# Kernel optimization log

Hardware: AMD Instinct MI355X
Metric: run time of the kernel (lower is better)

Reference implementation:

```python
import jax, jax.numpy as jnp
import numpy as np

H = 1024
F = 3584
E = 8
TOP_K = 2
B, S = 2, 1024


def setup_inputs() -> dict:
    key = jax.random.key(0)
    ks = jax.random.split(key, 5)
    scale_h = 1.0 / np.sqrt(H)
    scale_f = 1.0 / np.sqrt(F)
    return {
        "hidden_states": jax.random.normal(ks[0], (B, S, H), dtype=jnp.float32),
        "gate_w": jax.random.normal(ks[1], (H, E), dtype=jnp.float32) * scale_h,
        "w1": jax.random.normal(ks[2], (E, H, F), dtype=jnp.float32) * scale_h,
        "w3": jax.random.normal(ks[3], (E, H, F), dtype=jnp.float32) * scale_h,
        "w2": jax.random.normal(ks[4], (E, F, H), dtype=jnp.float32) * scale_f,
        "top_k": TOP_K,
    }


def reference(hidden_states, gate_w, w1, w3, w2, top_k):
    b, s, h = hidden_states.shape
    e = gate_w.shape[1]
    x = hidden_states.reshape(-1, h)  # [N, H]

    # Router: softmax over experts, top-k selection, renormalize (Mixtral).
    logits = x @ gate_w                             # [N, E]
    probs = jax.nn.softmax(logits, axis=-1)
    rw, sel = jax.lax.top_k(probs, top_k)           # [N, K]
    rw = rw / jnp.sum(rw, axis=-1, keepdims=True)

    # Dispatch/combine weights: combine[n, e] = sum_k rw[n,k] * (sel[n,k]==e).
    # This is the mathematical equivalent of moe_permute + weighted moe_unpermute.
    combine = jnp.sum(jax.nn.one_hot(sel, e, dtype=rw.dtype) * rw[..., None], axis=1)  # [N, E]

    # Grouped SwiGLU expert MLPs; loop over the small fixed expert count so the
    # [N, F] intermediate is materialized one expert at a time.
    out = jnp.zeros_like(x)
    for ei in range(e):
        hdn = jax.nn.silu(x @ w1[ei]) * (x @ w3[ei])  # [N, F]
        out = out + combine[:, ei:ei + 1] * (hdn @ w2[ei])
    return out.reshape(b, s, h)
```

## Files before the change

### kernel.cpp

```cpp
#include <hip/hip_runtime.h>
#include <hip/hip_bf16.h>

#define NTOK 2048
#define HD   1024
#define FD   3584
#define NE   8

#define BM 128
#define BN1 64
#define BN 128
#define BK 64
#define NIT1 (HD / BK)
#define KS2 4
#define KLEN2 (FD / KS2)
#define NIT2 (KLEN2 / BK)

typedef __attribute__((ext_vector_type(8))) short short8;
typedef __attribute__((ext_vector_type(4))) float f32x4;

__device__ __forceinline__ unsigned short f2bf(float f) {
    __hip_bfloat16 h = __float2bfloat16(f);
    union { __hip_bfloat16 h; unsigned short u; } c; c.h = h;
    return c.u;
}

typedef __attribute__((address_space(1))) const unsigned int g_cu32;
typedef __attribute__((address_space(3))) unsigned int l_u32;
__device__ __forceinline__ void gl16(const void* g, void* l) {
    __builtin_amdgcn_global_load_lds((g_cu32*)g, (l_u32*)(unsigned int)(size_t)l, 16, 0, 0);
}

__global__ void k_router(const float* __restrict__ x, const float* __restrict__ gw,
                         int* __restrict__ sel, float* __restrict__ selw,
                         int* __restrict__ counts) {
    int token = blockIdx.x * 4 + (threadIdx.x >> 6);
    int lane  = threadIdx.x & 63;
    if (token >= NTOK) return;
    const float* xr = x + (size_t)token * HD;
    float acc[NE];
#pragma unroll
    for (int e = 0; e < NE; e++) acc[e] = 0.f;
    for (int h = lane; h < HD; h += 64) {
        float xv = xr[h];
        const float4* g = (const float4*)(gw + (size_t)h * NE);
        float4 g0 = g[0], g1 = g[1];
        acc[0] += xv * g0.x; acc[1] += xv * g0.y; acc[2] += xv * g0.z; acc[3] += xv * g0.w;
        acc[4] += xv * g1.x; acc[5] += xv * g1.y; acc[6] += xv * g1.z; acc[7] += xv * g1.w;
    }
#pragma unroll
    for (int e = 0; e < NE; e++) {
#pragma unroll
        for (int off = 32; off >= 1; off >>= 1) acc[e] += __shfl_xor(acc[e], off, 64);
    }
    if (lane == 0) {
        float m = acc[0];
#pragma unroll
        for (int e = 1; e < NE; e++) m = fmaxf(m, acc[e]);
        float z[NE];
#pragma unroll
        for (int e = 0; e < NE; e++) z[e] = expf(acc[e] - m);
        int e0 = 0; float z0 = z[0];
#pragma unroll
        for (int e = 1; e < NE; e++) if (z[e] > z0) { z0 = z[e]; e0 = e; }
        int e1 = -1; float z1 = -1.f;
#pragma unroll
        for (int e = 0; e < NE; e++) if (e != e0 && z[e] > z1) { z1 = z[e]; e1 = e; }
        float s = z0 + z1;
        sel[token * 2 + 0] = e0; sel[token * 2 + 1] = e1;
        selw[token * 2 + 0] = z0 / s; selw[token * 2 + 1] = z1 / s;
        atomicAdd(&counts[e0], 1);
        atomicAdd(&counts[e1], 1);
    }
}

__global__ void k_scan(const int* __restrict__ counts, int* __restrict__ basep,
                       int* __restrict__ fillc) {
    if (threadIdx.x == 0 && blockIdx.x == 0) {
        int b = 0;
        for (int e = 0; e < NE; e++) { basep[e] = b; b += counts[e]; fillc[e] = 0; }
    }
}

__global__ void k_fill(const int* __restrict__ sel, const float* __restrict__ selw,
                       const int* __restrict__ basep, int* __restrict__ fillc,
                       int* __restrict__ rowmap, int* __restrict__ rowk,
                       float* __restrict__ roww) {
    int n = blockIdx.x * blockDim.x + threadIdx.x;
    if (n >= NTOK) return;
#pragma unroll
    for (int k = 0; k < 2; k++) {
        int e = sel[n * 2 + k];
        int p = atomicAdd(&fillc[e], 1);
        int g = basep[e] + p;
        rowmap[g] = n; rowk[g] = k; roww[g] = selw[n * 2 + k];
    }
}

__global__ void k_cvt(const float* __restrict__ x, unsigned short* __restrict__ xb) {
    size_t i = ((size_t)blockIdx.x * blockDim.x + threadIdx.x) * 8;
    float4 a = *(const float4*)(x + i);
    float4 b = *(const float4*)(x + i + 4);
    unsigned short p[8] __attribute__((aligned(16))) =
        { f2bf(a.x), f2bf(a.y), f2bf(a.z), f2bf(a.w),
          f2bf(b.x), f2bf(b.y), f2bf(b.z), f2bf(b.w) };
    *(uint4*)(xb + i) = *(uint4*)p;
}

__global__ void k_wt(const float* __restrict__ w, unsigned short* __restrict__ wt,
                     int K, int N) {
    __shared__ unsigned short tile[64][66];
    const int t = threadIdx.x;
    const float* src = w + (size_t)blockIdx.z * K * N + ((size_t)blockIdx.y * 64) * N + blockIdx.x * 64;
    {
        const int r = t >> 4;
        const int c4 = (t & 15) * 4;
#pragma unroll
        for (int i = 0; i < 4; i++) {
            const int kr = r + i * 16;
            float4 v = *(const float4*)(src + (size_t)kr * N + c4);
            unsigned short p[4] = { f2bf(v.x), f2bf(v.y), f2bf(v.z), f2bf(v.w) };
            *(unsigned int*)&tile[kr][c4]     = *(unsigned int*)&p[0];
            *(unsigned int*)&tile[kr][c4 + 2] = *(unsigned int*)&p[2];
        }
    }
    __syncthreads();
    unsigned short* dst = wt + (size_t)blockIdx.z * N * K + ((size_t)blockIdx.x * 64) * K + blockIdx.y * 64;
    const int n = t >> 3;
    const int kc = (t & 7) * 8;
#pragma unroll
    for (int i = 0; i < 2; i++) {
        const int nn = n + i * 32;
        unsigned short p[8] __attribute__((aligned(16)));
#pragma unroll
        for (int j = 0; j < 8; j++) p[j] = tile[kc + j][nn];
        *(uint4*)&dst[(size_t)nn * K + kc] = *(uint4*)p;
    }
}

__global__ __launch_bounds__(512, 4) void k_gemm1(
    const unsigned short* __restrict__ xb,
    const unsigned short* __restrict__ w1t, const unsigned short* __restrict__ w3t,
    const int* __restrict__ counts, const int* __restrict__ basep,
    const int* __restrict__ rowmap, unsigned short* __restrict__ act)
{
    const int e = blockIdx.z;
    const int nrows = counts[e];
    const int m0 = blockIdx.y * BM;
    if (m0 >= nrows) return;
    const int f0 = blockIdx.x * BN1;
    const int gbase = basep[e];

    __shared__ __align__(16) unsigned short At[2][BM][BK];
    __shared__ __align__(16) unsigned short B1[2][BN1][BK];
    __shared__ __align__(16) unsigned short B3[2][BN1][BK];

    const int t = threadIdx.x;
    const int lane = t & 63;
    const int w = t >> 6;
    const int wrm = w >> 1, wnn = w & 1;
    const int lr = lane >> 3;
    const int so = ((lane & 7) ^ lr) * 8;

    const unsigned short* asrc[2];
#pragma unroll
    for (int c = 0; c < 2; c++) {
        const int row = (w * 2 + c) * 8 + lr;
        const int tok = rowmap[gbase + min(m0 + row, nrows - 1)];
        asrc[c] = xb + (size_t)tok * HD + so;
    }
    const int brow = w * 8 + lr;
    const unsigned short* b1src = w1t + ((size_t)(e * FD + f0 + brow)) * HD + so;
    const unsigned short* b3src = w3t + ((size_t)(e * FD + f0 + brow)) * HD + so;

    f32x4 acc1[2][2], acc3[2][2];
#pragma unroll
    for (int i = 0; i < 2; i++)
#pragma unroll
        for (int j = 0; j < 2; j++) { acc1[i][j] = (f32x4)(0.f); acc3[i][j] = (f32x4)(0.f); }

    const int l15 = lane & 15;
    const int lhi = lane >> 4;
    const int rs = (l15 & 7) * 8;

#pragma unroll
    for (int c = 0; c < 2; c++) gl16(asrc[c], &At[0][(w * 2 + c) * 8][0]);
    gl16(b1src, &B1[0][w * 8][0]);
    gl16(b3src, &B3[0][w * 8][0]);

    for (int it = 0; it < NIT1; ++it) {
        const int cur = it & 1;
        if (it + 1 < NIT1) {
            const int kn = (it + 1) * BK;
#pragma unroll
            for (int c = 0; c < 2; c++) gl16(asrc[c] + kn, &At[cur ^ 1][(w * 2 + c) * 8][0]);
            gl16(b1src + kn, &B1[cur ^ 1][w * 8][0]);
            gl16(b3src + kn, &B3[cur ^ 1][w * 8][0]);
            asm volatile("s_waitcnt vmcnt(4)" ::: "memory");
        } else {
            asm volatile("s_waitcnt vmcnt(0)" ::: "memory");
        }
        __builtin_amdgcn_s_barrier();
#pragma unroll
        for (int kk = 0; kk < 2; kk++) {
            const int kc = (kk * 32 + lhi * 8) ^ rs;
            short8 af[2], b1f[2], b3f[2];
#pragma unroll
            for (int i = 0; i < 2; i++)
                af[i] = *(const short8*)&At[cur][wrm * 32 + i * 16 + l15][kc];
#pragma unroll
            for (int j = 0; j < 2; j++) {
                b1f[j] = *(const short8*)&B1[cur][wnn * 32 + j * 16 + l15][kc];
                b3f[j] = *(const short8*)&B3[cur][wnn * 32 + j * 16 + l15][kc];
            }
#pragma unroll
            for (int i = 0; i < 2; i++)
#pragma unroll
                for (int j = 0; j < 2; j++) {
                    acc1[i][j] = __builtin_amdgcn_mfma_f32_16x16x32_bf16(af[i], b1f[j], acc1[i][j], 0, 0, 0);
                    acc3[i][j] = __builtin_amdgcn_mfma_f32_16x16x32_bf16(af[i], b3f[j], acc3[i][j], 0, 0, 0);
                }
        }
        __builtin_amdgcn_s_barrier();
    }

    const int rbase = wrm * 32 + lhi * 4;
    const int cbase = f0 + wnn * 32 + l15;
#pragma unroll
    for (int i = 0; i < 2; i++) {
#pragma unroll
        for (int r = 0; r < 4; r++) {
            const int ml = rbase + i * 16 + r;
            if (m0 + ml < nrows) {
                const size_t rowoff = (size_t)(gbase + m0 + ml) * FD;
#pragma unroll
                for (int j = 0; j < 2; j++) {
                    float y1 = acc1[i][j][r];
                    float y3 = acc3[i][j][r];
                    float sv = (y1 / (1.f + __expf(-y1))) * y3;
                    act[rowoff + cbase + j * 16] = f2bf(sv);
                }
            }
        }
    }
}

__global__ __launch_bounds__(512, 4) void k_gemm2(
    const unsigned short* __restrict__ act,
    const unsigned short* __restrict__ w2t,
    const int* __restrict__ counts, const int* __restrict__ basep,
    const int* __restrict__ rowmap, const int* __restrict__ rowk,
    const float* __restrict__ roww, float* __restrict__ partial)
{
    const int z = blockIdx.z;
    const int e = z >> 2, ks = z & 3;
    const int nrows = counts[e];
    const int m0 = blockIdx.y * BM;
    if (m0 >= nrows) return;
    const int h0 = blockIdx.x * BN;
    const int gbase = basep[e];
    const int kbase = ks * KLEN2;

    __shared__ __align__(16) unsigned short At[2][BM][BK];
    __shared__ __align__(16) unsigned short Bt[2][BN][BK];

    const int t = threadIdx.x;
    const int lane = t & 63;
    const int w = t >> 6;
    const int wr = w >> 2, wn = w & 3;
    const int lr = lane >> 3;
    const int so = ((lane & 7) ^ lr) * 8;

    const unsigned short* asrc[2];
    const unsigned short* bsrc[2];
#pragma unroll
    for (int c = 0; c < 2; c++) {
        const int row = (w * 2 + c) * 8 + lr;
        asrc[c] = act + ((size_t)gbase + min(m0 + row, nrows - 1)) * FD + so + kbase;
        bsrc[c] = w2t + ((size_t)(e * HD + h0 + row)) * FD + so + kbase;
    }

    f32x4 acc[4][2];
#pragma unroll
    for (int i = 0; i < 4; i++)
#pragma unroll
        for (int j = 0; j < 2; j++) acc[i][j] = (f32x4)(0.f);

    const int l15 = lane & 15;
    const int lhi = lane >> 4;
    const int rs = (l15 & 7) * 8;

#pragma unroll
    for (int c = 0; c < 2; c++) {
        gl16(asrc[c], &At[0][(w * 2 + c) * 8][0]);
        gl16(bsrc[c], &Bt[0][(w * 2 + c) * 8][0]);
    }

    for (int it = 0; it < NIT2; ++it) {
        const int cur = it & 1;
        if (it + 1 < NIT2) {
            const int kn = (it + 1) * BK;
#pragma unroll
            for (int c = 0; c < 2; c++) {
                gl16(asrc[c] + kn, &At[cur ^ 1][(w * 2 + c) * 8][0]);
                gl16(bsrc[c] + kn, &Bt[cur ^ 1][(w * 2 + c) * 8][0]);
            }
            asm volatile("s_waitcnt vmcnt(4)" ::: "memory");
        } else {
            asm volatile("s_waitcnt vmcnt(0)" ::: "memory");
        }
        __builtin_amdgcn_s_barrier();
#pragma unroll
        for (int kk = 0; kk < 2; kk++) {
            const int kc = (kk * 32 + lhi * 8) ^ rs;
            short8 af[4], bf[2];
#pragma unroll
            for (int i = 0; i < 4; i++)
                af[i] = *(const short8*)&At[cur][wr * 64 + i * 16 + l15][kc];
#pragma unroll
            for (int j = 0; j < 2; j++)
                bf[j] = *(const short8*)&Bt[cur][wn * 32 + j * 16 + l15][kc];
#pragma unroll
            for (int i = 0; i < 4; i++)
#pragma unroll
                for (int j = 0; j < 2; j++)
                    acc[i][j] = __builtin_amdgcn_mfma_f32_16x16x32_bf16(af[i], bf[j], acc[i][j], 0, 0, 0);
        }
        __builtin_amdgcn_s_barrier();
    }

    const int rbase = wr * 64 + lhi * 4;
    const int cbase = h0 + wn * 32 + l15;
#pragma unroll
    for (int i = 0; i < 4; i++) {
#pragma unroll
        for (int r = 0; r < 4; r++) {
            const int ml = rbase + i * 16 + r;
            if (m0 + ml < nrows) {
                const int grow = gbase + m0 + ml;
                const int tok = rowmap[grow];
                const int slot = rowk[grow];
                const float wv = roww[grow];
                float* op = partial + (((size_t)slot * KS2 + ks) * NTOK + tok) * HD + cbase;
#pragma unroll
                for (int j = 0; j < 2; j++) op[j * 16] = acc[i][j][r] * wv;
            }
        }
    }
}

__global__ void k_combine(const float* __restrict__ partial, float* __restrict__ out) {
    size_t i = ((size_t)blockIdx.x * blockDim.x + threadIdx.x) * 4;
    const size_t st = (size_t)NTOK * HD;
    float4 o = *(const float4*)(partial + i);
#pragma unroll
    for (int s = 1; s < 2 * KS2; s++) {
        float4 v = *(const float4*)(partial + (size_t)s * st + i);
        o.x += v.x; o.y += v.y; o.z += v.z; o.w += v.w;
    }
    *(float4*)(out + i) = o;
}

extern "C" void kernel_launch(void* const* d_in, const int* in_sizes, int n_in,
                              void* d_out, int out_size, void* d_ws, size_t ws_size,
                              hipStream_t stream) {
    const float* x  = (const float*)d_in[0];
    const float* gw = (const float*)d_in[1];
    const float* w1 = (const float*)d_in[2];
    const float* w3 = (const float*)d_in[3];
    const float* w2 = (const float*)d_in[4];
    float* out = (float*)d_out;

    char* ws = (char*)d_ws;
    size_t off = 0;
    auto alloc = [&](size_t b) { char* p = ws + off; off += (b + 255) & ~(size_t)255; return p; };
    int*   sel    = (int*)  alloc((size_t)NTOK * 2 * 4);
    float* selw   = (float*)alloc((size_t)NTOK * 2 * 4);
    int*   counts = (int*)  alloc(NE * 4);
    int*   basep  = (int*)  alloc(NE * 4);
    int*   fillc  = (int*)  alloc(NE * 4);
    int*   rowmap = (int*)  alloc((size_t)NTOK * 2 * 4);
    int*   rowk   = (int*)  alloc((size_t)NTOK * 2 * 4);
    float* roww   = (float*)alloc((size_t)NTOK * 2 * 4);
    unsigned short* xb  = (unsigned short*)alloc((size_t)NTOK * HD * 2);
    unsigned short* act = (unsigned short*)alloc((size_t)NTOK * 2 * FD * 2);
    unsigned short* w1t = (unsigned short*)alloc((size_t)NE * HD * FD * 2);
    unsigned short* w3t = (unsigned short*)alloc((size_t)NE * HD * FD * 2);
    unsigned short* w2t = (unsigned short*)alloc((size_t)NE * HD * FD * 2);
    float* partial = (float*)w1t;

    hipMemsetAsync(counts, 0, NE * 4, stream);
    k_wt<<<dim3(FD / 64, HD / 64, NE), 256, 0, stream>>>(w1, w1t, HD, FD);
    k_wt<<<dim3(FD / 64, HD / 64, NE), 256, 0, stream>>>(w3, w3t, HD, FD);
    k_wt<<<dim3(HD / 64, FD / 64, NE), 256, 0, stream>>>(w2, w2t, FD, HD);
    k_cvt<<<(NTOK * HD) / (256 * 8), 256, 0, stream>>>(x, xb);
    k_router<<<NTOK / 4, 256, 0, stream>>>(x, gw, sel, selw, counts);
    k_scan<<<1, 64, 0, stream>>>(counts, basep, fillc);
    k_fill<<<NTOK / 256, 256, 0, stream>>>(sel, selw, basep, fillc, rowmap, rowk, roww);
    k_gemm1<<<dim3(FD / BN1, NTOK / BM, NE), 512, 0, stream>>>(xb, w1t, w3t, counts, basep, rowmap, act);
    k_gemm2<<<dim3(HD / BN, NTOK / BM, NE * KS2), 512, 0, stream>>>(act, w2t, counts, basep, rowmap, rowk, roww, partial);
    k_combine<<<(NTOK * HD) / (256 * 4), 256, 0, stream>>>(partial, out);
}
```

Measured before the change: 340.0 us.

## Retile both MoE GEMMs for 256-thread blocks, halve split-K, fuse weight transposes

The three weight transpose/convert launches are merged into one kernel that picks w1, w3 or w2 from blockIdx.z. gemm1 now runs 256-thread blocks, with each wave covering 64 rows instead of 32. That gives it more MFMA work per wave and more reuse of each A/B fragment, at the cost of more accumulator registers. gemm2 uses a 64-row M tile, 64-column per-wave N tiles and split-K of 2 instead of 4. This halves the partial buffers that are written and then summed in the combine kernel, but each block gets a longer K loop and there are fewer blocks to spread across the device.

```diff
diff --git a/kernel.cpp b/kernel.cpp
--- a/kernel.cpp
+++ b/kernel.cpp
@@ -8,10 +8,11 @@
 
 #define BM 128
 #define BN1 64
+#define BM2 64
 #define BN 128
 #define BK 64
 #define NIT1 (HD / BK)
-#define KS2 4
+#define KS2 2
 #define KLEN2 (FD / KS2)
 #define NIT2 (KLEN2 / BK)
 
@@ -106,11 +107,32 @@
     *(uint4*)(xb + i) = *(uint4*)p;
 }
 
-__global__ void k_wt(const float* __restrict__ w, unsigned short* __restrict__ wt,
-                     int K, int N) {
+__global__ void k_wt3(const float* __restrict__ w1, const float* __restrict__ w3,
+                      const float* __restrict__ w2,
+                      unsigned short* __restrict__ w1t, unsigned short* __restrict__ w3t,
+                      unsigned short* __restrict__ w2t) {
     __shared__ unsigned short tile[64][66];
+    const int z = blockIdx.z;
+    int K, N, tx, ty;
+    const float* src;
+    unsigned short* dst;
+    if (z < 16) {
+        K = HD; N = FD;
+        const int e = z & 7;
+        src = (z < 8 ? w1 : w3) + (size_t)e * K * N;
+        dst = (z < 8 ? w1t : w3t) + (size_t)e * N * K;
+        tx = blockIdx.x % (FD / 64); ty = blockIdx.x / (FD / 64);
+    } else {
+        K = FD; N = HD;
+        const int e = z - 16;
+        src = w2 + (size_t)e * K * N;
+        dst = w2t + (size_t)e * N * K;
+        tx = blockIdx.x % (HD / 64); ty = blockIdx.x / (HD / 64);
+    }
+    src += (size_t)(ty * 64) * N + tx * 64;
+    dst += (size_t)(tx * 64) * K + ty * 64;
+
     const int t = threadIdx.x;
-    const float* src = w + (size_t)blockIdx.z * K * N + ((size_t)blockIdx.y * 64) * N + blockIdx.x * 64;
     {
         const int r = t >> 4;
         const int c4 = (t & 15) * 4;
@@ -124,7 +146,6 @@
         }
     }
     __syncthreads();
-    unsigned short* dst = wt + (size_t)blockIdx.z * N * K + ((size_t)blockIdx.x * 64) * K + blockIdx.y * 64;
     const int n = t >> 3;
     const int kc = (t & 7) * 8;
 #pragma unroll
@@ -137,7 +158,7 @@
     }
 }
 
-__global__ __launch_bounds__(512, 4) void k_gemm1(
+__global__ __launch_bounds__(256, 2) void k_gemm1(
     const unsigned short* __restrict__ xb,
     const unsigned short* __restrict__ w1t, const unsigned short* __restrict__ w3t,
     const int* __restrict__ counts, const int* __restrict__ basep,
@@ -161,20 +182,25 @@
     const int lr = lane >> 3;
     const int so = ((lane & 7) ^ lr) * 8;
 
-    const unsigned short* asrc[2];
+    const unsigned short* asrc[4];
+#pragma unroll
+    for (int c = 0; c < 4; c++) {
+        const int row = (w * 4 + c) * 8 + lr;
+        const int tok = rowmap[gbase + min(m0 + row, nrows - 1)];
+        asrc[c] = xb + (size_t)tok * HD + so;
+    }
+    const unsigned short* b1src[2];
+    const unsigned short* b3src[2];
 #pragma unroll
     for (int c = 0; c < 2; c++) {
         const int row = (w * 2 + c) * 8 + lr;
-        const int tok = rowmap[gbase + min(m0 + row, nrows - 1)];
-        asrc[c] = xb + (size_t)tok * HD + so;
-    }
-    const int brow = w * 8 + lr;
-    const unsigned short* b1src = w1t + ((size_t)(e * FD + f0 + brow)) * HD + so;
-    const unsigned short* b3src = w3t + ((size_t)(e * FD + f0 + brow)) * HD + so;
-
-    f32x4 acc1[2][2], acc3[2][2];
-#pragma unroll
-    for (int i = 0; i < 2; i++)
+        b1src[c] = w1t + ((size_t)(e * FD + f0 + row)) * HD + so;
+        b3src[c] = w3t + ((size_t)(e * FD + f0 + row)) * HD + so;
+    }
+
+    f32x4 acc1[4][2], acc3[4][2];
+#pragma unroll
+    for (int i = 0; i < 4; i++)
 #pragma unroll
         for (int j = 0; j < 2; j++) { acc1[i][j] = (f32x4)(0.f); acc3[i][j] = (f32x4)(0.f); }
 
@@ -183,19 +209,25 @@
     const int rs = (l15 & 7) * 8;
 
 #pragma unroll
-    for (int c = 0; c < 2; c++) gl16(asrc[c], &At[0][(w * 2 + c) * 8][0]);
-    gl16(b1src, &B1[0][w * 8][0]);
-    gl16(b3src, &B3[0][w * 8][0]);
+    for (int c = 0; c < 4; c++) gl16(asrc[c], &At[0][(w * 4 + c) * 8][0]);
+#pragma unroll
+    for (int c = 0; c < 2; c++) {
+        gl16(b1src[c], &B1[0][(w * 2 + c) * 8][0]);
+        gl16(b3src[c], &B3[0][(w * 2 + c) * 8][0]);
+    }
 
     for (int it = 0; it < NIT1; ++it) {
         const int cur = it & 1;
         if (it + 1 < NIT1) {
             const int kn = (it + 1) * BK;
 #pragma unroll
-            for (int c = 0; c < 2; c++) gl16(asrc[c] + kn, &At[cur ^ 1][(w * 2 + c) * 8][0]);
-            gl16(b1src + kn, &B1[cur ^ 1][w * 8][0]);
-            gl16(b3src + kn, &B3[cur ^ 1][w * 8][0]);
-            asm volatile("s_waitcnt vmcnt(4)" ::: "memory");
+            for (int c = 0; c < 4; c++) gl16(asrc[c] + kn, &At[cur ^ 1][(w * 4 + c) * 8][0]);
+#pragma unroll
+            for (int c = 0; c < 2; c++) {
+                gl16(b1src[c] + kn, &B1[cur ^ 1][(w * 2 + c) * 8][0]);
+                gl16(b3src[c] + kn, &B3[cur ^ 1][(w * 2 + c) * 8][0]);
+            }
+            asm volatile("s_waitcnt vmcnt(8)" ::: "memory");
         } else {
             asm volatile("s_waitcnt vmcnt(0)" ::: "memory");
         }
@@ -203,17 +235,17 @@
 #pragma unroll
         for (int kk = 0; kk < 2; kk++) {
             const int kc = (kk * 32 + lhi * 8) ^ rs;
-            short8 af[2], b1f[2], b3f[2];
-#pragma unroll
-            for (int i = 0; i < 2; i++)
-                af[i] = *(const short8*)&At[cur][wrm * 32 + i * 16 + l15][kc];
+            short8 af[4], b1f[2], b3f[2];
+#pragma unroll
+            for (int i = 0; i < 4; i++)
+                af[i] = *(const short8*)&At[cur][wrm * 64 + i * 16 + l15][kc];
 #pragma unroll
             for (int j = 0; j < 2; j++) {
                 b1f[j] = *(const short8*)&B1[cur][wnn * 32 + j * 16 + l15][kc];
                 b3f[j] = *(const short8*)&B3[cur][wnn * 32 + j * 16 + l15][kc];
             }
 #pragma unroll
-            for (int i = 0; i < 2; i++)
+            for (int i = 0; i < 4; i++)
 #pragma unroll
                 for (int j = 0; j < 2; j++) {
                     acc1[i][j] = __builtin_amdgcn_mfma_f32_16x16x32_bf16(af[i], b1f[j], acc1[i][j], 0, 0, 0);
@@ -223,10 +255,10 @@
         __builtin_amdgcn_s_barrier();
     }
 
-    const int rbase = wrm * 32 + lhi * 4;
+    const int rbase = wrm * 64 + lhi * 4;
     const int cbase = f0 + wnn * 32 + l15;
 #pragma unroll
-    for (int i = 0; i < 2; i++) {
+    for (int i = 0; i < 4; i++) {
 #pragma unroll
         for (int r = 0; r < 4; r++) {
             const int ml = rbase + i * 16 + r;
@@ -244,7 +276,7 @@
     }
 }
 
-__global__ __launch_bounds__(512, 4) void k_gemm2(
+__global__ __launch_bounds__(256, 4) void k_gemm2(
     const unsigned short* __restrict__ act,
     const unsigned short* __restrict__ w2t,
     const int* __restrict__ counts, const int* __restrict__ basep,
@@ -252,59 +284,61 @@
     const float* __restrict__ roww, float* __restrict__ partial)
 {
     const int z = blockIdx.z;
-    const int e = z >> 2, ks = z & 3;
+    const int e = z >> 1, ks = z & 1;
     const int nrows = counts[e];
-    const int m0 = blockIdx.y * BM;
+    const int m0 = blockIdx.y * BM2;
     if (m0 >= nrows) return;
     const int h0 = blockIdx.x * BN;
     const int gbase = basep[e];
     const int kbase = ks * KLEN2;
 
-    __shared__ __align__(16) unsigned short At[2][BM][BK];
+    __shared__ __align__(16) unsigned short At[2][BM2][BK];
     __shared__ __align__(16) unsigned short Bt[2][BN][BK];
 
     const int t = threadIdx.x;
     const int lane = t & 63;
     const int w = t >> 6;
-    const int wr = w >> 2, wn = w & 3;
+    const int wr2 = w >> 1, wn2 = w & 1;
     const int lr = lane >> 3;
     const int so = ((lane & 7) ^ lr) * 8;
 
     const unsigned short* asrc[2];
-    const unsigned short* bsrc[2];
 #pragma unroll
     for (int c = 0; c < 2; c++) {
         const int row = (w * 2 + c) * 8 + lr;
         asrc[c] = act + ((size_t)gbase + min(m0 + row, nrows - 1)) * FD + so + kbase;
+    }
+    const unsigned short* bsrc[4];
+#pragma unroll
+    for (int c = 0; c < 4; c++) {
+        const int row = (w * 4 + c) * 8 + lr;
         bsrc[c] = w2t + ((size_t)(e * HD + h0 + row)) * FD + so + kbase;
     }
 
-    f32x4 acc[4][2];
-#pragma unroll
-    for (int i = 0; i < 4; i++)
-#pragma unroll
-        for (int j = 0; j < 2; j++) acc[i][j] = (f32x4)(0.f);
+    f32x4 acc[2][4];
+#pragma unroll
+    for (int i = 0; i < 2; i++)
+#pragma unroll
+        for (int j = 0; j < 4; j++) acc[i][j] = (f32x4)(0.f);
 
     const int l15 = lane & 15;
     const int lhi = lane >> 4;
     const int rs = (l15 & 7) * 8;
 
 #pragma unroll
-    for (int c = 0; c < 2; c++) {
-        gl16(asrc[c], &At[0][(w * 2 + c) * 8][0]);
-        gl16(bsrc[c], &Bt[0][(w * 2 + c) * 8][0]);
-    }
+    for (int c = 0; c < 2; c++) gl16(asrc[c], &At[0][(w * 2 + c) * 8][0]);
+#pragma unroll
+    for (int c = 0; c < 4; c++) gl16(bsrc[c], &Bt[0][(w * 4 + c) * 8][0]);
 
     for (int it = 0; it < NIT2; ++it) {
         const int cur = it & 1;
         if (it + 1 < NIT2) {
             const int kn = (it + 1) * BK;
 #pragma unroll
-            for (int c = 0; c < 2; c++) {
-                gl16(asrc[c] + kn, &At[cur ^ 1][(w * 2 + c) * 8][0]);
-                gl16(bsrc[c] + kn, &Bt[cur ^ 1][(w * 2 + c) * 8][0]);
-            }
-            asm volatile("s_waitcnt vmcnt(4)" ::: "memory");
+            for (int c = 0; c < 2; c++) gl16(asrc[c] + kn, &At[cur ^ 1][(w * 2 + c) * 8][0]);
+#pragma unroll
+            for (int c = 0; c < 4; c++) gl16(bsrc[c] + kn, &Bt[cur ^ 1][(w * 4 + c) * 8][0]);
+            asm volatile("s_waitcnt vmcnt(6)" ::: "memory");
         } else {
             asm volatile("s_waitcnt vmcnt(0)" ::: "memory");
         }
@@ -312,26 +346,26 @@
 #pragma unroll
         for (int kk = 0; kk < 2; kk++) {
             const int kc = (kk * 32 + lhi * 8) ^ rs;
-            short8 af[4], bf[2];
-#pragma unroll
-            for (int i = 0; i < 4; i++)
-                af[i] = *(const short8*)&At[cur][wr * 64 + i * 16 + l15][kc];
-#pragma unroll
-            for (int j = 0; j < 2; j++)
-                bf[j] = *(const short8*)&Bt[cur][wn * 32 + j * 16 + l15][kc];
-#pragma unroll
-            for (int i = 0; i < 4; i++)
-#pragma unroll
-                for (int j = 0; j < 2; j++)
+            short8 af[2], bf[4];
+#pragma unroll
+            for (int i = 0; i < 2; i++)
+                af[i] = *(const short8*)&At[cur][wr2 * 32 + i * 16 + l15][kc];
+#pragma unroll
+            for (int j = 0; j < 4; j++)
+                bf[j] = *(const short8*)&Bt[cur][wn2 * 64 + j * 16 + l15][kc];
+#pragma unroll
+            for (int i = 0; i < 2; i++)
+#pragma unroll
+                for (int j = 0; j < 4; j++)
                     acc[i][j] = __builtin_amdgcn_mfma_f32_16x16x32_bf16(af[i], bf[j], acc[i][j], 0, 0, 0);
         }
         __builtin_amdgcn_s_barrier();
     }
 
-    const int rbase = wr * 64 + lhi * 4;
-    const int cbase = h0 + wn * 32 + l15;
-#pragma unroll
-    for (int i = 0; i < 4; i++) {
+    const int rbase = wr2 * 32 + lhi * 4;
+    const int cbase = h0 + wn2 * 64 + l15;
+#pragma unroll
+    for (int i = 0; i < 2; i++) {
 #pragma unroll
         for (int r = 0; r < 4; r++) {
             const int ml = rbase + i * 16 + r;
@@ -342,7 +376,7 @@
                 const float wv = roww[grow];
                 float* op = partial + (((size_t)slot * KS2 + ks) * NTOK + tok) * HD + cbase;
 #pragma unroll
-                for (int j = 0; j < 2; j++) op[j * 16] = acc[i][j][r] * wv;
+                for (int j = 0; j < 4; j++) op[j * 16] = acc[i][j][r] * wv;
             }
         }
     }
@@ -389,14 +423,12 @@
     float* partial = (float*)w1t;
 
     hipMemsetAsync(counts, 0, NE * 4, stream);
-    k_wt<<<dim3(FD / 64, HD / 64, NE), 256, 0, stream>>>(w1, w1t, HD, FD);
-    k_wt<<<dim3(FD / 64, HD / 64, NE), 256, 0, stream>>>(w3, w3t, HD, FD);
-    k_wt<<<dim3(HD / 64, FD / 64, NE), 256, 0, stream>>>(w2, w2t, FD, HD);
+    k_wt3<<<dim3(896, 1, 24), 256, 0, stream>>>(w1, w3, w2, w1t, w3t, w2t);
     k_cvt<<<(NTOK * HD) / (256 * 8), 256, 0, stream>>>(x, xb);
     k_router<<<NTOK / 4, 256, 0, stream>>>(x, gw, sel, selw, counts);
     k_scan<<<1, 64, 0, stream>>>(counts, basep, fillc);
     k_fill<<<NTOK / 256, 256, 0, stream>>>(sel, selw, basep, fillc, rowmap, rowk, roww);
-    k_gemm1<<<dim3(FD / BN1, NTOK / BM, NE), 512, 0, stream>>>(xb, w1t, w3t, counts, basep, rowmap, act);
-    k_gemm2<<<dim3(HD / BN, NTOK / BM, NE * KS2), 512, 0, stream>>>(act, w2t, counts, basep, rowmap, rowk, roww, partial);
+    k_gemm1<<<dim3(FD / BN1, NTOK / BM, NE), 256, 0, stream>>>(xb, w1t, w3t, counts, basep, rowmap, act);
+    k_gemm2<<<dim3(HD / BN, NTOK / BM2, NE * KS2), 256, 0, stream>>>(act, w2t, counts, basep, rowmap, rowk, roww, partial);
     k_combine<<<(NTOK * HD) / (256 * 4), 256, 0, stream>>>(partial, out);
 }
```

Result: faster. 330.6 us (-2.8%).
